# Performance work log

Measured on AMD Instinct MI355X. Metric: run time of the kernel, lower is better.

Reference implementation:

```python
import jax, jax.numpy as jnp
import numpy as np

L_SEQ = 32768
H_FEAT = 512
P_STATE = 256  # state_size // 2 (conj_sym)
LOG_DT_MIN, LOG_DT_MAX = np.log(1e-3), np.log(1e-1)


def setup_inputs() -> dict:
    key = jax.random.key(0)
    ks = jax.random.split(key, 7)
    input_sequence = jax.random.normal(ks[0], (L_SEQ, H_FEAT), dtype=jnp.float32)
    # eigenvalue real parts must be negative for stability (HiPPO-LegS-like)
    lambda_real = -jax.random.uniform(ks[1], (P_STATE,), minval=0.1, maxval=1.0, dtype=jnp.float32)
    lambda_imag = jax.random.normal(ks[2], (P_STATE,), dtype=jnp.float32) * float(np.pi)
    b = jax.random.normal(ks[3], (P_STATE, H_FEAT, 2), dtype=jnp.float32) / np.sqrt(H_FEAT)
    c = jax.random.normal(ks[4], (H_FEAT, P_STATE, 2), dtype=jnp.float32) / np.sqrt(P_STATE)
    d = jax.random.normal(ks[5], (H_FEAT,), dtype=jnp.float32)
    # log-timestep init in [log(1e-3), log(1e-1)] as in init_log_steps
    delta = (LOG_DT_MIN + jax.random.uniform(ks[6], (P_STATE, 1), dtype=jnp.float32)
             * (LOG_DT_MAX - LOG_DT_MIN))
    return {"input_sequence": input_sequence, "lambda_real": lambda_real,
            "lambda_imag": lambda_imag, "b": b, "c": c, "d": d, "delta": delta}


def _binop(e_i, e_j):
    A_i, b_i = e_i
    A_j, b_j = e_j
    return A_j * A_i, A_j * b_i + b_j


def reference(input_sequence, lambda_real, lambda_imag, b, c, d, delta):
    # assemble complex parameters (stored as real [..., 2])
    Lam = lambda_real + 1j * lambda_imag            # [P]
    B = b[..., 0] + 1j * b[..., 1]                  # [P, H]
    C = c[..., 0] + 1j * c[..., 1]                  # [H, P]
    step = jnp.exp(delta[:, 0])                     # step_rescale = 1.0
    # bilinear discretization
    BL = 1.0 / (1.0 - (step / 2.0) * Lam)
    Lam_bar = BL * (1.0 + (step / 2.0) * Lam)       # [P]
    B_bar = (BL * step)[:, None] * B                # [P, H]
    # input projection: Bu[l] = B_bar @ u[l]
    Bu = jnp.einsum('lh,ph->lp', input_sequence.astype(Lam_bar.dtype), B_bar)  # [L, P]
    L = input_sequence.shape[0]
    Lam_el = jnp.broadcast_to(Lam_bar, (L, Lam_bar.shape[0]))
    _, xs = jax.lax.associative_scan(_binop, (Lam_el, Bu))  # xs: [L, P] complex states
    # output projection (conj_sym => factor 2, real part)
    ys = 2.0 * jnp.einsum('lp,hp->lh', xs, C).real  # [L, H]
    return ys + d * input_sequence
```

## Files before the change

kernel.cpp:

```cpp
#include <hip/hip_runtime.h>
#include <cstddef>

#define L_SEQ 32768
#define H_FEAT 512
#define P_STATE 256
#define N2 512
#define CS 32
#define NCH (L_SEQ / CS)

typedef __bf16 bf16x8 __attribute__((ext_vector_type(8)));
typedef float f32x4 __attribute__((ext_vector_type(4)));

#define GLDS16(g, l) __builtin_amdgcn_global_load_lds( \
    (const __attribute__((address_space(1))) void*)(g), \
    (__attribute__((address_space(3))) void*)(l), 16, 0, 0)

__device__ __forceinline__ unsigned bf_rne(float x) {
    unsigned u = __float_as_uint(x);
    return (u + 0x7fffu + ((u >> 16) & 1u)) >> 16;
}
__device__ __forceinline__ float bf_f(unsigned bits) {
    return __uint_as_float(bits << 16);
}

__global__ __launch_bounds__(256) void param_kernel(
    const float* __restrict__ lr, const float* __restrict__ li,
    const float* __restrict__ b,  const float* __restrict__ c,
    const float* __restrict__ delta,
    ushort* __restrict__ W_hi, ushort* __restrict__ W_lo,
    ushort* __restrict__ C2_hi, ushort* __restrict__ C2_lo,
    float2* __restrict__ Abar)
{
    int tid = blockIdx.x * blockDim.x + threadIdx.x;

    {
        int p = tid >> 9;
        int h = tid & 511;
        float step = expf(delta[p]);
        float zr = 0.5f * step * lr[p];
        float zi = 0.5f * step * li[p];
        float dr = 1.0f - zr, di = -zi;
        float den = dr * dr + di * di;
        float blr = dr / den, bli = -di / den;
        float bbr = blr * step, bbi = bli * step;
        float b0 = b[((size_t)(p * H_FEAT + h)) * 2 + 0];
        float b1 = b[((size_t)(p * H_FEAT + h)) * 2 + 1];
        float vr = bbr * b0 - bbi * b1;
        float vi = bbr * b1 + bbi * b0;
        unsigned hr = bf_rne(vr), hl = bf_rne(vr - bf_f(hr));
        unsigned ir = bf_rne(vi), il = bf_rne(vi - bf_f(ir));
        size_t o0 = (size_t)(2 * p) * H_FEAT + h;
        size_t o1 = (size_t)(2 * p + 1) * H_FEAT + h;
        W_hi[o0] = (ushort)hr; W_lo[o0] = (ushort)hl;
        W_hi[o1] = (ushort)ir; W_lo[o1] = (ushort)il;
    }

    {
        int h2 = tid >> 8;
        int p2 = tid & 255;
        float c0 =  2.0f * c[((size_t)(h2 * P_STATE + p2)) * 2 + 0];
        float c1 = -2.0f * c[((size_t)(h2 * P_STATE + p2)) * 2 + 1];
        unsigned h0 = bf_rne(c0), l0 = bf_rne(c0 - bf_f(h0));
        unsigned h1 = bf_rne(c1), l1 = bf_rne(c1 - bf_f(h1));
        size_t o0 = (size_t)h2 * N2 + 2 * p2;
        C2_hi[o0] = (ushort)h0;     C2_lo[o0] = (ushort)l0;
        C2_hi[o0 + 1] = (ushort)h1; C2_lo[o0 + 1] = (ushort)l1;
    }

    if (tid < P_STATE) {
        int p = tid;
        float step = expf(delta[p]);
        float zr = 0.5f * step * lr[p];
        float zi = 0.5f * step * li[p];
        float dr = 1.0f - zr, di = -zi;
        float den = dr * dr + di * di;
        float blr = dr / den, bli = -di / den;
        float nr = 1.0f + zr, ni = zi;
        Abar[p] = make_float2(blr * nr - bli * ni, blr * ni + bli * nr);
    }
}

__global__ __launch_bounds__(256, 2) void gemm1(
    const float* __restrict__ A,
    const ushort* __restrict__ Bhi, const ushort* __restrict__ Blo,
    float* __restrict__ C)
{
    __shared__ ushort As_hi[128 * 32], As_lo[128 * 32];
    __shared__ ushort Bs_hi[256 * 32], Bs_lo[256 * 32];
    const int tid = threadIdx.x;
    const int ln = tid & 63, wv = tid >> 6;
    const int bm = blockIdx.y * 128, bn = blockIdx.x * 256;
    const int m = ln & 15, q = ln >> 4;
    const int wr = (wv >> 1) * 64, wc = (wv & 1) * 128;

    f32x4 acc[4][8] = {};

    for (int k0 = 0; k0 < 512; k0 += 32) {
#pragma unroll
        for (int s = 0; s < 8; s++) {
            int t = wv * 8 + s;
            int ch = t & 15;
            int row = ch * 16 + (ln >> 2);
            const ushort* src = (t < 16 ? Bhi : Blo)
                                + (size_t)(bn + row) * 512 + k0 + (ln & 3) * 8;
            ushort* dst = (t < 16 ? Bs_hi : Bs_lo) + ch * 512 + ln * 8;
            GLDS16(src, dst);
        }
#pragma unroll
        for (int r = 0; r < 4; r++) {
            int idx = tid + r * 256;
            int row = idx >> 3;
            int c4 = (idx & 7) << 2;
            const float4 v = *(const float4*)(A + (size_t)(bm + row) * 512 + k0 + c4);
            unsigned u0 = __float_as_uint(v.x), u1 = __float_as_uint(v.y);
            unsigned u2 = __float_as_uint(v.z), u3 = __float_as_uint(v.w);
            unsigned hi01 = (u0 >> 16) | (u1 & 0xffff0000u);
            unsigned hi23 = (u2 >> 16) | (u3 & 0xffff0000u);
            float d0 = v.x - __uint_as_float(u0 & 0xffff0000u);
            float d1 = v.y - __uint_as_float(u1 & 0xffff0000u);
            float d2 = v.z - __uint_as_float(u2 & 0xffff0000u);
            float d3 = v.w - __uint_as_float(u3 & 0xffff0000u);
            unsigned lo01 = (__float_as_uint(d0) >> 16) | (__float_as_uint(d1) & 0xffff0000u);
            unsigned lo23 = (__float_as_uint(d2) >> 16) | (__float_as_uint(d3) & 0xffff0000u);
            *(uint2*)(As_hi + row * 32 + c4) = make_uint2(hi01, hi23);
            *(uint2*)(As_lo + row * 32 + c4) = make_uint2(lo01, lo23);
        }
        __syncthreads();

        bf16x8 ah[4], al[4];
#pragma unroll
        for (int i = 0; i < 4; i++) {
            ah[i] = *(const bf16x8*)(As_hi + (wr + i * 16 + m) * 32 + q * 8);
            al[i] = *(const bf16x8*)(As_lo + (wr + i * 16 + m) * 32 + q * 8);
        }
#pragma unroll
        for (int j = 0; j < 8; j++) {
            bf16x8 bh = *(const bf16x8*)(Bs_hi + (wc + j * 16 + m) * 32 + q * 8);
            bf16x8 bl = *(const bf16x8*)(Bs_lo + (wc + j * 16 + m) * 32 + q * 8);
#pragma unroll
            for (int i = 0; i < 4; i++)
                acc[i][j] = __builtin_amdgcn_mfma_f32_16x16x32_bf16(ah[i], bh, acc[i][j], 0, 0, 0);
#pragma unroll
            for (int i = 0; i < 4; i++)
                acc[i][j] = __builtin_amdgcn_mfma_f32_16x16x32_bf16(al[i], bh, acc[i][j], 0, 0, 0);
#pragma unroll
            for (int i = 0; i < 4; i++)
                acc[i][j] = __builtin_amdgcn_mfma_f32_16x16x32_bf16(ah[i], bl, acc[i][j], 0, 0, 0);
        }
        __syncthreads();
    }

#pragma unroll
    for (int i = 0; i < 4; i++)
#pragma unroll
        for (int j = 0; j < 8; j++)
#pragma unroll
            for (int r = 0; r < 4; r++) {
                int row = bm + wr + i * 16 + q * 4 + r;
                int col = bn + wc + j * 16 + m;
                C[(size_t)row * 512 + col] = acc[i][j][r];
            }
}

__global__ __launch_bounds__(256, 2) void gemm2(
    const unsigned* __restrict__ Xp,
    const ushort* __restrict__ Bhi, const ushort* __restrict__ Blo,
    float* __restrict__ Cout, const float* __restrict__ U,
    const float* __restrict__ dvec)
{
    __shared__ ushort As_hi[128 * 32], As_lo[128 * 32];
    __shared__ ushort Bs_hi[256 * 32], Bs_lo[256 * 32];
    const int tid = threadIdx.x;
    const int ln = tid & 63, wv = tid >> 6;
    const int bm = blockIdx.y * 128, bn = blockIdx.x * 256;
    const int m = ln & 15, q = ln >> 4;
    const int wr = (wv >> 1) * 64, wc = (wv & 1) * 128;

    f32x4 acc[4][8] = {};

    for (int k0 = 0; k0 < 512; k0 += 32) {
#pragma unroll
        for (int s = 0; s < 8; s++) {
            int t = wv * 8 + s;
            int ch = t & 15;
            int row = ch * 16 + (ln >> 2);
            const ushort* src = (t < 16 ? Bhi : Blo)
                                + (size_t)(bn + row) * 512 + k0 + (ln & 3) * 8;
            ushort* dst = (t < 16 ? Bs_hi : Bs_lo) + ch * 512 + ln * 8;
            GLDS16(src, dst);
        }
#pragma unroll
        for (int r = 0; r < 4; r++) {
            int idx = tid + r * 256;
            int row = idx >> 3;
            int c4 = (idx & 7) << 2;
            const uint4 v = *(const uint4*)(Xp + (size_t)(bm + row) * 512 + k0 + c4);
            unsigned hi01 = (v.x >> 16) | (v.y & 0xffff0000u);
            unsigned hi23 = (v.z >> 16) | (v.w & 0xffff0000u);
            unsigned lo01 = (v.x & 0xffffu) | (v.y << 16);
            unsigned lo23 = (v.z & 0xffffu) | (v.w << 16);
            *(uint2*)(As_hi + row * 32 + c4) = make_uint2(hi01, hi23);
            *(uint2*)(As_lo + row * 32 + c4) = make_uint2(lo01, lo23);
        }
        __syncthreads();

        bf16x8 ah[4], al[4];
#pragma unroll
        for (int i = 0; i < 4; i++) {
            ah[i] = *(const bf16x8*)(As_hi + (wr + i * 16 + m) * 32 + q * 8);
            al[i] = *(const bf16x8*)(As_lo + (wr + i * 16 + m) * 32 + q * 8);
        }
#pragma unroll
        for (int j = 0; j < 8; j++) {
            bf16x8 bh = *(const bf16x8*)(Bs_hi + (wc + j * 16 + m) * 32 + q * 8);
            bf16x8 bl = *(const bf16x8*)(Bs_lo + (wc + j * 16 + m) * 32 + q * 8);
#pragma unroll
            for (int i = 0; i < 4; i++)
                acc[i][j] = __builtin_amdgcn_mfma_f32_16x16x32_bf16(ah[i], bh, acc[i][j], 0, 0, 0);
#pragma unroll
            for (int i = 0; i < 4; i++)
                acc[i][j] = __builtin_amdgcn_mfma_f32_16x16x32_bf16(al[i], bh, acc[i][j], 0, 0, 0);
#pragma unroll
            for (int i = 0; i < 4; i++)
                acc[i][j] = __builtin_amdgcn_mfma_f32_16x16x32_bf16(ah[i], bl, acc[i][j], 0, 0, 0);
        }
        __syncthreads();
    }

#pragma unroll
    for (int i = 0; i < 4; i++)
#pragma unroll
        for (int j = 0; j < 8; j++) {
            int col = bn + wc + j * 16 + m;
            float dv = dvec[col];
#pragma unroll
            for (int r = 0; r < 4; r++) {
                int row = bm + wr + i * 16 + q * 4 + r;
                Cout[(size_t)row * 512 + col] =
                    acc[i][j][r] + dv * U[(size_t)row * 512 + col];
            }
        }
}

__global__ __launch_bounds__(256) void scan_pass1(
    const float4* __restrict__ Bu4, const float2* __restrict__ Abar,
    float2* __restrict__ ends)
{
    int tid = blockIdx.x * 256 + threadIdx.x;
    int chunk = tid >> 7;
    int pq = tid & 127;
    float2 A0 = Abar[2 * pq], A1 = Abar[2 * pq + 1];
    float2 s0 = make_float2(0.f, 0.f), s1 = make_float2(0.f, 0.f);
    const float4* ptr = Bu4 + (size_t)chunk * CS * 128 + pq;
#pragma unroll 8
    for (int i = 0; i < CS; i++) {
        float4 v = ptr[(size_t)i * 128];
        float sr0 = fmaf(A0.x, s0.x, fmaf(-A0.y, s0.y, v.x));
        float si0 = fmaf(A0.x, s0.y, fmaf(A0.y, s0.x, v.y));
        float sr1 = fmaf(A1.x, s1.x, fmaf(-A1.y, s1.y, v.z));
        float si1 = fmaf(A1.x, s1.y, fmaf(A1.y, s1.x, v.w));
        s0 = make_float2(sr0, si0); s1 = make_float2(sr1, si1);
    }
    ends[(size_t)(2 * pq) * NCH + chunk] = s0;
    ends[(size_t)(2 * pq + 1) * NCH + chunk] = s1;
}

__global__ __launch_bounds__(1024) void scan_pass2(
    const float2* __restrict__ ends, const float2* __restrict__ Abar,
    float2* __restrict__ carries)
{
    __shared__ float2 sA[NCH];
    __shared__ float2 sB[NCH];
    int p = blockIdx.x;
    int t = threadIdx.x;

    float2 a = Abar[p];
#pragma unroll
    for (int i = 0; i < 5; i++) {
        float nr = a.x * a.x - a.y * a.y;
        float ni = 2.f * a.x * a.y;
        a = make_float2(nr, ni);
    }
    float2 A = a;
    float2 bv = ends[(size_t)p * NCH + t];
    sA[t] = A; sB[t] = bv;
    __syncthreads();

    for (int off = 1; off < NCH; off <<= 1) {
        float2 pa, pb;
        bool act = (t >= off);
        if (act) { pa = sA[t - off]; pb = sB[t - off]; }
        __syncthreads();
        if (act) {
            float2 nA = make_float2(A.x * pa.x - A.y * pa.y,
                                    A.x * pa.y + A.y * pa.x);
            float2 nB = make_float2(fmaf(A.x, pb.x, fmaf(-A.y, pb.y, bv.x)),
                                    fmaf(A.x, pb.y, fmaf(A.y, pb.x, bv.y)));
            A = nA; bv = nB;
            sA[t] = A; sB[t] = bv;
        }
        __syncthreads();
    }

    float2 carry = (t == 0) ? make_float2(0.f, 0.f) : sB[t - 1];
    carries[(size_t)p * NCH + t] = carry;
}

__global__ __launch_bounds__(256) void scan_pass3(
    float4* __restrict__ Bu4, const float2* __restrict__ Abar,
    const float2* __restrict__ carries)
{
    int tid = blockIdx.x * 256 + threadIdx.x;
    int chunk = tid >> 7;
    int pq = tid & 127;
    float2 A0 = Abar[2 * pq], A1 = Abar[2 * pq + 1];
    float2 s0 = carries[(size_t)(2 * pq) * NCH + chunk];
    float2 s1 = carries[(size_t)(2 * pq + 1) * NCH + chunk];
    float4* ptr = Bu4 + (size_t)chunk * CS * 128 + pq;
#pragma unroll 8
    for (int i = 0; i < CS; i++) {
        float4 v = ptr[(size_t)i * 128];
        float sr0 = fmaf(A0.x, s0.x, fmaf(-A0.y, s0.y, v.x));
        float si0 = fmaf(A0.x, s0.y, fmaf(A0.y, s0.x, v.y));
        float sr1 = fmaf(A1.x, s1.x, fmaf(-A1.y, s1.y, v.z));
        float si1 = fmaf(A1.x, s1.y, fmaf(A1.y, s1.x, v.w));
        s0 = make_float2(sr0, si0); s1 = make_float2(sr1, si1);
        unsigned r0h = bf_rne(sr0), r0l = __float_as_uint(sr0 - bf_f(r0h)) >> 16;
        unsigned i0h = bf_rne(si0), i0l = __float_as_uint(si0 - bf_f(i0h)) >> 16;
        unsigned r1h = bf_rne(sr1), r1l = __float_as_uint(sr1 - bf_f(r1h)) >> 16;
        unsigned i1h = bf_rne(si1), i1l = __float_as_uint(si1 - bf_f(i1h)) >> 16;
        uint4 w = make_uint4((r0h << 16) | r0l, (i0h << 16) | i0l,
                             (r1h << 16) | r1l, (i1h << 16) | i1l);
        *(uint4*)(ptr + (size_t)i * 128) = w;
    }
}

extern "C" void kernel_launch(void* const* d_in, const int* in_sizes, int n_in,
                              void* d_out, int out_size, void* d_ws, size_t ws_size,
                              hipStream_t stream) {
    const float* u     = (const float*)d_in[0];
    const float* lr    = (const float*)d_in[1];
    const float* li    = (const float*)d_in[2];
    const float* b     = (const float*)d_in[3];
    const float* c     = (const float*)d_in[4];
    const float* dvec  = (const float*)d_in[5];
    const float* delta = (const float*)d_in[6];
    float* out = (float*)d_out;

    char* p = (char*)d_ws;
    float*  Bu      = (float*)p;   p += (size_t)L_SEQ * N2 * 4;
    float2* ends    = (float2*)p;  p += (size_t)P_STATE * NCH * 8;
    float2* carries = (float2*)p;  p += (size_t)P_STATE * NCH * 8;
    ushort* W_hi    = (ushort*)p;  p += (size_t)N2 * H_FEAT * 2;
    ushort* W_lo    = (ushort*)p;  p += (size_t)N2 * H_FEAT * 2;
    ushort* C2_hi   = (ushort*)p;  p += (size_t)H_FEAT * N2 * 2;
    ushort* C2_lo   = (ushort*)p;  p += (size_t)H_FEAT * N2 * 2;
    float2* Abar    = (float2*)p;  p += (size_t)P_STATE * 8;

    param_kernel<<<(P_STATE * H_FEAT) / 256, 256, 0, stream>>>(
        lr, li, b, c, delta, W_hi, W_lo, C2_hi, C2_lo, Abar);

    {
        dim3 grid(N2 / 256, L_SEQ / 128);
        gemm1<<<grid, 256, 0, stream>>>(u, W_hi, W_lo, Bu);
    }

    scan_pass1<<<NCH * 128 / 256, 256, 0, stream>>>(
        (const float4*)Bu, Abar, ends);
    scan_pass2<<<P_STATE, NCH, 0, stream>>>(ends, Abar, carries);
    scan_pass3<<<NCH * 128 / 256, 256, 0, stream>>>(
        (float4*)Bu, Abar, carries);

    {
        dim3 grid(H_FEAT / 256, L_SEQ / 128);
        gemm2<<<grid, 256, 0, stream>>>((const unsigned*)Bu, C2_hi, C2_lo,
                                        out, u, dvec);
    }
}
```

Measured before the change: 254.0 us.

## Fold scan carry fix-up into gemm2 prologue and drop third scan pass

Pass 1 of the chunked scan now writes the local (zero-initialised) chunk states back to Bu. The separate third pass that re-read Bu to apply chunk carries is removed. Instead, gemm2 applies the correction x = local + A^(r+1) * carry while staging its A tile, using a precomputed table of powers of A and carries transposed to [chunk][p]. It also does the hi/lo bf16 split there. This saves one full read/write sweep of the L×512 state buffer and a kernel launch. In exchange, gemm2's load path does extra loads and FMAs, and hi is now split by truncation rather than round-to-nearest.

```diff
diff --git a/kernel.cpp b/kernel.cpp
--- a/kernel.cpp
+++ b/kernel.cpp
@@ -22,6 +22,9 @@
 __device__ __forceinline__ float bf_f(unsigned bits) {
     return __uint_as_float(bits << 16);
 }
+__device__ __forceinline__ float2 cmul(float2 a, float2 b) {
+    return make_float2(a.x * b.x - a.y * b.y, a.x * b.y + a.y * b.x);
+}
 
 __global__ __launch_bounds__(256) void param_kernel(
     const float* __restrict__ lr, const float* __restrict__ li,
@@ -29,7 +32,7 @@
     const float* __restrict__ delta,
     ushort* __restrict__ W_hi, ushort* __restrict__ W_lo,
     ushort* __restrict__ C2_hi, ushort* __restrict__ C2_lo,
-    float2* __restrict__ Abar)
+    float2* __restrict__ Abar, float2* __restrict__ Apw)
 {
     int tid = blockIdx.x * blockDim.x + threadIdx.x;
 
@@ -67,8 +70,9 @@
         C2_hi[o0 + 1] = (ushort)h1; C2_lo[o0 + 1] = (ushort)l1;
     }
 
-    if (tid < P_STATE) {
-        int p = tid;
+    if (tid < CS * P_STATE) {
+        int r = tid >> 8;
+        int p = tid & 255;
         float step = expf(delta[p]);
         float zr = 0.5f * step * lr[p];
         float zi = 0.5f * step * li[p];
@@ -76,7 +80,16 @@
         float den = dr * dr + di * di;
         float blr = dr / den, bli = -di / den;
         float nr = 1.0f + zr, ni = zi;
-        Abar[p] = make_float2(blr * nr - bli * ni, blr * ni + bli * nr);
+        float2 ab = make_float2(blr * nr - bli * ni, blr * ni + bli * nr);
+        if (r == 0) Abar[p] = ab;
+        int e = r + 1;
+        float2 res = make_float2(1.f, 0.f), base = ab;
+        while (e) {
+            if (e & 1) res = cmul(res, base);
+            base = cmul(base, base);
+            e >>= 1;
+        }
+        Apw[r * P_STATE + p] = res;
     }
 }
 
@@ -163,18 +176,30 @@
 }
 
 __global__ __launch_bounds__(256, 2) void gemm2(
-    const unsigned* __restrict__ Xp,
+    const float* __restrict__ Xs,
+    const float2* __restrict__ Apw,
+    const float2* __restrict__ carr,
     const ushort* __restrict__ Bhi, const ushort* __restrict__ Blo,
     float* __restrict__ Cout, const float* __restrict__ U,
     const float* __restrict__ dvec)
 {
     __shared__ ushort As_hi[128 * 32], As_lo[128 * 32];
     __shared__ ushort Bs_hi[256 * 32], Bs_lo[256 * 32];
+    __shared__ __align__(16) float cLds[4 * 512];
     const int tid = threadIdx.x;
     const int ln = tid & 63, wv = tid >> 6;
     const int bm = blockIdx.y * 128, bn = blockIdx.x * 256;
     const int m = ln & 15, q = ln >> 4;
     const int wr = (wv >> 1) * 64, wc = (wv & 1) * 128;
+
+    if (tid < 256) {
+#pragma unroll
+        for (int k = 0; k < 4; k++) {
+            float2 cv = carr[(size_t)(blockIdx.y * 4 + k) * P_STATE + tid];
+            ((float2*)cLds)[k * 256 + tid] = cv;
+        }
+    }
+    __syncthreads();
 
     f32x4 acc[4][8] = {};
 
@@ -194,11 +219,24 @@
             int idx = tid + r * 256;
             int row = idx >> 3;
             int c4 = (idx & 7) << 2;
-            const uint4 v = *(const uint4*)(Xp + (size_t)(bm + row) * 512 + k0 + c4);
-            unsigned hi01 = (v.x >> 16) | (v.y & 0xffff0000u);
-            unsigned hi23 = (v.z >> 16) | (v.w & 0xffff0000u);
-            unsigned lo01 = (v.x & 0xffffu) | (v.y << 16);
-            unsigned lo23 = (v.z & 0xffffu) | (v.w << 16);
+            const float4 v = *(const float4*)(Xs + (size_t)(bm + row) * 512 + k0 + c4);
+            int p0 = (k0 + c4) >> 1;
+            const float4 w = *(const float4*)(Apw + (size_t)(row & 31) * P_STATE + p0);
+            const float4 cv = *(const float4*)(cLds + (row >> 5) * 512 + 2 * p0);
+            float x0 = fmaf(w.x, cv.x, fmaf(-w.y, cv.y, v.x));
+            float y0 = fmaf(w.x, cv.y, fmaf(w.y, cv.x, v.y));
+            float x1 = fmaf(w.z, cv.z, fmaf(-w.w, cv.w, v.z));
+            float y1 = fmaf(w.z, cv.w, fmaf(w.w, cv.z, v.w));
+            unsigned u0 = __float_as_uint(x0), u1 = __float_as_uint(y0);
+            unsigned u2 = __float_as_uint(x1), u3 = __float_as_uint(y1);
+            unsigned hi01 = (u0 >> 16) | (u1 & 0xffff0000u);
+            unsigned hi23 = (u2 >> 16) | (u3 & 0xffff0000u);
+            float d0 = x0 - __uint_as_float(u0 & 0xffff0000u);
+            float d1 = y0 - __uint_as_float(u1 & 0xffff0000u);
+            float d2 = x1 - __uint_as_float(u2 & 0xffff0000u);
+            float d3 = y1 - __uint_as_float(u3 & 0xffff0000u);
+            unsigned lo01 = (__float_as_uint(d0) >> 16) | (__float_as_uint(d1) & 0xffff0000u);
+            unsigned lo23 = (__float_as_uint(d2) >> 16) | (__float_as_uint(d3) & 0xffff0000u);
             *(uint2*)(As_hi + row * 32 + c4) = make_uint2(hi01, hi23);
             *(uint2*)(As_lo + row * 32 + c4) = make_uint2(lo01, lo23);
         }
@@ -243,7 +281,7 @@
 }
 
 __global__ __launch_bounds__(256) void scan_pass1(
-    const float4* __restrict__ Bu4, const float2* __restrict__ Abar,
+    float4* __restrict__ Bu4, const float2* __restrict__ Abar,
     float2* __restrict__ ends)
 {
     int tid = blockIdx.x * 256 + threadIdx.x;
@@ -251,71 +289,6 @@
     int pq = tid & 127;
     float2 A0 = Abar[2 * pq], A1 = Abar[2 * pq + 1];
     float2 s0 = make_float2(0.f, 0.f), s1 = make_float2(0.f, 0.f);
-    const float4* ptr = Bu4 + (size_t)chunk * CS * 128 + pq;
-#pragma unroll 8
-    for (int i = 0; i < CS; i++) {
-        float4 v = ptr[(size_t)i * 128];
-        float sr0 = fmaf(A0.x, s0.x, fmaf(-A0.y, s0.y, v.x));
-        float si0 = fmaf(A0.x, s0.y, fmaf(A0.y, s0.x, v.y));
-        float sr1 = fmaf(A1.x, s1.x, fmaf(-A1.y, s1.y, v.z));
-        float si1 = fmaf(A1.x, s1.y, fmaf(A1.y, s1.x, v.w));
-        s0 = make_float2(sr0, si0); s1 = make_float2(sr1, si1);
-    }
-    ends[(size_t)(2 * pq) * NCH + chunk] = s0;
-    ends[(size_t)(2 * pq + 1) * NCH + chunk] = s1;
-}
-
-__global__ __launch_bounds__(1024) void scan_pass2(
-    const float2* __restrict__ ends, const float2* __restrict__ Abar,
-    float2* __restrict__ carries)
-{
-    __shared__ float2 sA[NCH];
-    __shared__ float2 sB[NCH];
-    int p = blockIdx.x;
-    int t = threadIdx.x;
-
-    float2 a = Abar[p];
-#pragma unroll
-    for (int i = 0; i < 5; i++) {
-        float nr = a.x * a.x - a.y * a.y;
-        float ni = 2.f * a.x * a.y;
-        a = make_float2(nr, ni);
-    }
-    float2 A = a;
-    float2 bv = ends[(size_t)p * NCH + t];
-    sA[t] = A; sB[t] = bv;
-    __syncthreads();
-
-    for (int off = 1; off < NCH; off <<= 1) {
-        float2 pa, pb;
-        bool act = (t >= off);
-        if (act) { pa = sA[t - off]; pb = sB[t - off]; }
-        __syncthreads();
-        if (act) {
-            float2 nA = make_float2(A.x * pa.x - A.y * pa.y,
-                                    A.x * pa.y + A.y * pa.x);
-            float2 nB = make_float2(fmaf(A.x, pb.x, fmaf(-A.y, pb.y, bv.x)),
-                                    fmaf(A.x, pb.y, fmaf(A.y, pb.x, bv.y)));
-            A = nA; bv = nB;
-            sA[t] = A; sB[t] = bv;
-        }
-        __syncthreads();
-    }
-
-    float2 carry = (t == 0) ? make_float2(0.f, 0.f) : sB[t - 1];
-    carries[(size_t)p * NCH + t] = carry;
-}
-
-__global__ __launch_bounds__(256) void scan_pass3(
-    float4* __restrict__ Bu4, const float2* __restrict__ Abar,
-    const float2* __restrict__ carries)
-{
-    int tid = blockIdx.x * 256 + threadIdx.x;
-    int chunk = tid >> 7;
-    int pq = tid & 127;
-    float2 A0 = Abar[2 * pq], A1 = Abar[2 * pq + 1];
-    float2 s0 = carries[(size_t)(2 * pq) * NCH + chunk];
-    float2 s1 = carries[(size_t)(2 * pq + 1) * NCH + chunk];
     float4* ptr = Bu4 + (size_t)chunk * CS * 128 + pq;
 #pragma unroll 8
     for (int i = 0; i < CS; i++) {
@@ -325,14 +298,51 @@
         float sr1 = fmaf(A1.x, s1.x, fmaf(-A1.y, s1.y, v.z));
         float si1 = fmaf(A1.x, s1.y, fmaf(A1.y, s1.x, v.w));
         s0 = make_float2(sr0, si0); s1 = make_float2(sr1, si1);
-        unsigned r0h = bf_rne(sr0), r0l = __float_as_uint(sr0 - bf_f(r0h)) >> 16;
-        unsigned i0h = bf_rne(si0), i0l = __float_as_uint(si0 - bf_f(i0h)) >> 16;
-        unsigned r1h = bf_rne(sr1), r1l = __float_as_uint(sr1 - bf_f(r1h)) >> 16;
-        unsigned i1h = bf_rne(si1), i1l = __float_as_uint(si1 - bf_f(i1h)) >> 16;
-        uint4 w = make_uint4((r0h << 16) | r0l, (i0h << 16) | i0l,
-                             (r1h << 16) | r1l, (i1h << 16) | i1l);
-        *(uint4*)(ptr + (size_t)i * 128) = w;
-    }
+        ptr[(size_t)i * 128] = make_float4(sr0, si0, sr1, si1);
+    }
+    ends[(size_t)(2 * pq) * NCH + chunk] = s0;
+    ends[(size_t)(2 * pq + 1) * NCH + chunk] = s1;
+}
+
+__global__ __launch_bounds__(1024) void scan_pass2(
+    const float2* __restrict__ ends, const float2* __restrict__ Abar,
+    float2* __restrict__ carries)
+{
+    __shared__ float2 sA[NCH];
+    __shared__ float2 sB[NCH];
+    int p = blockIdx.x;
+    int t = threadIdx.x;
+
+    float2 a = Abar[p];
+#pragma unroll
+    for (int i = 0; i < 5; i++) {
+        float nr = a.x * a.x - a.y * a.y;
+        float ni = 2.f * a.x * a.y;
+        a = make_float2(nr, ni);
+    }
+    float2 A = a;
+    float2 bv = ends[(size_t)p * NCH + t];
+    sA[t] = A; sB[t] = bv;
+    __syncthreads();
+
+    for (int off = 1; off < NCH; off <<= 1) {
+        float2 pa, pb;
+        bool act = (t >= off);
+        if (act) { pa = sA[t - off]; pb = sB[t - off]; }
+        __syncthreads();
+        if (act) {
+            float2 nA = make_float2(A.x * pa.x - A.y * pa.y,
+                                    A.x * pa.y + A.y * pa.x);
+            float2 nB = make_float2(fmaf(A.x, pb.x, fmaf(-A.y, pb.y, bv.x)),
+                                    fmaf(A.x, pb.y, fmaf(A.y, pb.x, bv.y)));
+            A = nA; bv = nB;
+            sA[t] = A; sB[t] = bv;
+        }
+        __syncthreads();
+    }
+
+    float2 carry = (t == 0) ? make_float2(0.f, 0.f) : sB[t - 1];
+    carries[(size_t)t * P_STATE + p] = carry;
 }
 
 extern "C" void kernel_launch(void* const* d_in, const int* in_sizes, int n_in,
@@ -356,9 +366,10 @@
     ushort* C2_hi   = (ushort*)p;  p += (size_t)H_FEAT * N2 * 2;
     ushort* C2_lo   = (ushort*)p;  p += (size_t)H_FEAT * N2 * 2;
     float2* Abar    = (float2*)p;  p += (size_t)P_STATE * 8;
+    float2* Apw     = (float2*)p;  p += (size_t)CS * P_STATE * 8;
 
     param_kernel<<<(P_STATE * H_FEAT) / 256, 256, 0, stream>>>(
-        lr, li, b, c, delta, W_hi, W_lo, C2_hi, C2_lo, Abar);
+        lr, li, b, c, delta, W_hi, W_lo, C2_hi, C2_lo, Abar, Apw);
 
     {
         dim3 grid(N2 / 256, L_SEQ / 128);
@@ -366,14 +377,12 @@
     }
 
     scan_pass1<<<NCH * 128 / 256, 256, 0, stream>>>(
-        (const float4*)Bu, Abar, ends);
+        (float4*)Bu, Abar, ends);
     scan_pass2<<<P_STATE, NCH, 0, stream>>>(ends, Abar, carries);
-    scan_pass3<<<NCH * 128 / 256, 256, 0, stream>>>(
-        (float4*)Bu, Abar, carries);
 
     {
         dim3 grid(H_FEAT / 256, L_SEQ / 128);
-        gemm2<<<grid, 256, 0, stream>>>((const unsigned*)Bu, C2_hi, C2_lo,
+        gemm2<<<grid, 256, 0, stream>>>(Bu, Apw, carries, C2_hi, C2_lo,
                                         out, u, dvec);
     }
 }
```

Result: slower. 266.7 us (+5.0%).
